# Kernel optimization log

Measured on AMD Instinct MI355X. Metric: run time of the kernel, lower is better.

## Reference

```python
import jax, jax.numpy as jnp
import numpy as np

BIAS = (1, 1)  # from init_kwargs

def setup_inputs() -> dict:
    key = jax.random.key(0)
    k1, k2 = jax.random.split(key)
    B, L = 32, 2048
    c = jax.random.normal(k1, (B, L), dtype=jnp.float32)
    y = jax.random.randint(k2, (B, L), 0, 2, dtype=jnp.int32)
    return {"c": c, "y": y}

def reference(c, y):
    # Faithful BP-MLL loss:
    # L = mean_i  (1 / (|Y_i|^b0 * |Ybar_i|^b1)) * sum_{k in Y_i, l in Ybar_i} exp(c_l - c_k)
    yf = (y == 1).astype(c.dtype)          # [B, L] positive-label mask
    y_bar = (y != 1).astype(c.dtype)       # [B, L] negative-label mask
    y_norm = jnp.sum(yf, axis=1) ** BIAS[0]
    y_bar_norm = jnp.sum(y_bar, axis=1) ** BIAS[1]
    # exp_matrix[b, k, l] = exp(c[b, l] - c[b, k]); masked pairwise sum
    exp_matrix = jnp.exp(c[:, None, :] - c[:, :, None])  # [B, L, L]
    pair = jnp.einsum('bk,bl,bkl->b', yf, y_bar, exp_matrix)
    return jnp.mean(pair / (y_norm * y_bar_norm))
```

## Files before the change

### kernel.cpp

```cpp
#include <hip/hip_runtime.h>


#define B_BATCH 32
#define L_LEN   2048

__global__ __launch_bounds__(256) void bpmll_row_kernel(
    const float* __restrict__ c,
    const int*   __restrict__ y,
    float*       __restrict__ row_out)
{
    const int b   = blockIdx.x;
    const int tid = threadIdx.x;
    const float* crow = c + (size_t)b * L_LEN;
    const int*   yrow = y + (size_t)b * L_LEN;

    float s_pos = 0.f;
    float s_neg = 0.f;
    float n_pos = 0.f;

    #pragma unroll
    for (int base = 0; base < L_LEN; base += 256 * 4) {
        const int i = base + tid * 4;
        const float4 cv = *reinterpret_cast<const float4*>(crow + i);
        const int4   yv = *reinterpret_cast<const int4*>(yrow + i);
        const float cc[4] = {cv.x, cv.y, cv.z, cv.w};
        const int   yy[4] = {yv.x, yv.y, yv.z, yv.w};
        #pragma unroll
        for (int j = 0; j < 4; ++j) {
            const bool pos = (yy[j] == 1);
            const float e = __expf(pos ? -cc[j] : cc[j]);
            if (pos) { s_pos += e; n_pos += 1.f; }
            else     { s_neg += e; }
        }
    }

    #pragma unroll
    for (int off = 32; off > 0; off >>= 1) {
        s_pos += __shfl_down(s_pos, off);
        s_neg += __shfl_down(s_neg, off);
        n_pos += __shfl_down(n_pos, off);
    }

    __shared__ float sm[3][4];
    const int wave = tid >> 6;
    const int lane = tid & 63;
    if (lane == 0) { sm[0][wave] = s_pos; sm[1][wave] = s_neg; sm[2][wave] = n_pos; }
    __syncthreads();

    if (tid == 0) {
        const float sp = sm[0][0] + sm[0][1] + sm[0][2] + sm[0][3];
        const float sn = sm[1][0] + sm[1][1] + sm[1][2] + sm[1][3];
        const float np = sm[2][0] + sm[2][1] + sm[2][2] + sm[2][3];
        const float nn = (float)L_LEN - np;
        row_out[b] = (sp * sn) / (np * nn);
    }
}

__global__ __launch_bounds__(64) void bpmll_final_kernel(
    const float* __restrict__ row_out,
    float*       __restrict__ out)
{
    const int tid = threadIdx.x;
    float v = (tid < B_BATCH) ? row_out[tid] : 0.f;
    #pragma unroll
    for (int off = 32; off > 0; off >>= 1) v += __shfl_down(v, off);
    if (tid == 0) out[0] = v * (1.0f / (float)B_BATCH);
}

extern "C" void kernel_launch(void* const* d_in, const int* in_sizes, int n_in,
                              void* d_out, int out_size, void* d_ws, size_t ws_size,
                              hipStream_t stream)
{
    const float* c = (const float*)d_in[0];
    const int*   y = (const int*)d_in[1];
    float* row = (float*)d_ws;
    float* out = (float*)d_out;

    bpmll_row_kernel<<<B_BATCH, 256, 0, stream>>>(c, y, row);
    bpmll_final_kernel<<<1, 64, 0, stream>>>(row, out);
}
```

Baseline: 56.06 us.

## Fuse row and final reduction into a single one-block kernel

Measured after the change: 60.17 us. 7.3% more time.

```diff
diff --git a/kernel.cpp b/kernel.cpp
--- a/kernel.cpp
+++ b/kernel.cpp
@@ -3,68 +3,70 @@
 
 #define B_BATCH 32
 #define L_LEN   2048
+#define NTHREADS 1024
+#define NWAVES  (NTHREADS / 64)
+#define ROWS_PER_WAVE (B_BATCH / NWAVES)
 
-__global__ __launch_bounds__(256) void bpmll_row_kernel(
+__global__ __launch_bounds__(NTHREADS) void bpmll_fused_kernel(
     const float* __restrict__ c,
     const int*   __restrict__ y,
-    float*       __restrict__ row_out)
+    float*       __restrict__ out)
 {
-    const int b   = blockIdx.x;
-    const int tid = threadIdx.x;
-    const float* crow = c + (size_t)b * L_LEN;
-    const int*   yrow = y + (size_t)b * L_LEN;
+    const int tid  = threadIdx.x;
+    const int wave = tid >> 6;
+    const int lane = tid & 63;
 
-    float s_pos = 0.f;
-    float s_neg = 0.f;
-    float n_pos = 0.f;
+    float acc = 0.f;
 
     #pragma unroll
-    for (int base = 0; base < L_LEN; base += 256 * 4) {
-        const int i = base + tid * 4;
-        const float4 cv = *reinterpret_cast<const float4*>(crow + i);
-        const int4   yv = *reinterpret_cast<const int4*>(yrow + i);
-        const float cc[4] = {cv.x, cv.y, cv.z, cv.w};
-        const int   yy[4] = {yv.x, yv.y, yv.z, yv.w};
+    for (int r = 0; r < ROWS_PER_WAVE; ++r) {
+        const int b = wave * ROWS_PER_WAVE + r;
+        const float* crow = c + (size_t)b * L_LEN;
+        const int*   yrow = y + (size_t)b * L_LEN;
+
+        float s_pos = 0.f;
+        float s_neg = 0.f;
+        float n_pos = 0.f;
+
         #pragma unroll
-        for (int j = 0; j < 4; ++j) {
-            const bool pos = (yy[j] == 1);
-            const float e = __expf(pos ? -cc[j] : cc[j]);
-            if (pos) { s_pos += e; n_pos += 1.f; }
-            else     { s_neg += e; }
+        for (int base = 0; base < L_LEN; base += 64 * 4) {
+            const int i = base + lane * 4;
+            const float4 cv = *reinterpret_cast<const float4*>(crow + i);
+            const int4   yv = *reinterpret_cast<const int4*>(yrow + i);
+            const float cc[4] = {cv.x, cv.y, cv.z, cv.w};
+            const int   yy[4] = {yv.x, yv.y, yv.z, yv.w};
+            #pragma unroll
+            for (int j = 0; j < 4; ++j) {
+                const bool pos = (yy[j] == 1);
+                const float e = __expf(pos ? -cc[j] : cc[j]);
+                if (pos) { s_pos += e; n_pos += 1.f; }
+                else     { s_neg += e; }
+            }
+        }
+
+        #pragma unroll
+        for (int off = 32; off > 0; off >>= 1) {
+            s_pos += __shfl_down(s_pos, off);
+            s_neg += __shfl_down(s_neg, off);
+            n_pos += __shfl_down(n_pos, off);
+        }
+
+        if (lane == 0) {
+            const float nn = (float)L_LEN - n_pos;
+            acc += (s_pos * s_neg) / (n_pos * nn);
         }
     }
 
-    #pragma unroll
-    for (int off = 32; off > 0; off >>= 1) {
-        s_pos += __shfl_down(s_pos, off);
-        s_neg += __shfl_down(s_neg, off);
-        n_pos += __shfl_down(n_pos, off);
-    }
-
-    __shared__ float sm[3][4];
-    const int wave = tid >> 6;
-    const int lane = tid & 63;
-    if (lane == 0) { sm[0][wave] = s_pos; sm[1][wave] = s_neg; sm[2][wave] = n_pos; }
+    __shared__ float sm[NWAVES];
+    if (lane == 0) sm[wave] = acc;
     __syncthreads();
 
     if (tid == 0) {
-        const float sp = sm[0][0] + sm[0][1] + sm[0][2] + sm[0][3];
-        const float sn = sm[1][0] + sm[1][1] + sm[1][2] + sm[1][3];
-        const float np = sm[2][0] + sm[2][1] + sm[2][2] + sm[2][3];
-        const float nn = (float)L_LEN - np;
-        row_out[b] = (sp * sn) / (np * nn);
+        float v = 0.f;
+        #pragma unroll
+        for (int w = 0; w < NWAVES; ++w) v += sm[w];
+        out[0] = v * (1.0f / (float)B_BATCH);
     }
-}
-
-__global__ __launch_bounds__(64) void bpmll_final_kernel(
-    const float* __restrict__ row_out,
-    float*       __restrict__ out)
-{
-    const int tid = threadIdx.x;
-    float v = (tid < B_BATCH) ? row_out[tid] : 0.f;
-    #pragma unroll
-    for (int off = 32; off > 0; off >>= 1) v += __shfl_down(v, off);
-    if (tid == 0) out[0] = v * (1.0f / (float)B_BATCH);
 }
 
 extern "C" void kernel_launch(void* const* d_in, const int* in_sizes, int n_in,
@@ -73,9 +75,7 @@
 {
     const float* c = (const float*)d_in[0];
     const int*   y = (const int*)d_in[1];
-    float* row = (float*)d_ws;
     float* out = (float*)d_out;
 
-    bpmll_row_kernel<<<B_BATCH, 256, 0, stream>>>(c, y, row);
-    bpmll_final_kernel<<<1, 64, 0, stream>>>(row, out);
+    bpmll_fused_kernel<<<1, NTHREADS, 0, stream>>>(c, y, out);
 }
```

## Fuse per-row and final reduction into one kernel with flag spin-wait

Applied to the files above, without the earlier changes.

After: 55.59 us. No clear change (-0.8%).

```diff
diff --git a/kernel.cpp b/kernel.cpp
--- a/kernel.cpp
+++ b/kernel.cpp
@@ -1,13 +1,17 @@
 #include <hip/hip_runtime.h>
+#include <stdint.h>
 
 
 #define B_BATCH 32
 #define L_LEN   2048
+#define NTHREADS 256
+#define MAGIC   0x5ca1ab1eu
 
-__global__ __launch_bounds__(256) void bpmll_row_kernel(
+__global__ __launch_bounds__(NTHREADS) void bpmll_onepass_kernel(
     const float* __restrict__ c,
     const int*   __restrict__ y,
-    float*       __restrict__ row_out)
+    float*       __restrict__ out,
+    uint32_t*    __restrict__ ws)
 {
     const int b   = blockIdx.x;
     const int tid = threadIdx.x;
@@ -18,13 +22,17 @@
     float s_neg = 0.f;
     float n_pos = 0.f;
 
+    float4 cv[2]; int4 yv[2];
     #pragma unroll
-    for (int base = 0; base < L_LEN; base += 256 * 4) {
-        const int i = base + tid * 4;
-        const float4 cv = *reinterpret_cast<const float4*>(crow + i);
-        const int4   yv = *reinterpret_cast<const int4*>(yrow + i);
-        const float cc[4] = {cv.x, cv.y, cv.z, cv.w};
-        const int   yy[4] = {yv.x, yv.y, yv.z, yv.w};
+    for (int it = 0; it < 2; ++it) {
+        const int i = it * NTHREADS * 4 + tid * 4;
+        cv[it] = *reinterpret_cast<const float4*>(crow + i);
+        yv[it] = *reinterpret_cast<const int4*>(yrow + i);
+    }
+    #pragma unroll
+    for (int it = 0; it < 2; ++it) {
+        const float cc[4] = {cv[it].x, cv[it].y, cv[it].z, cv[it].w};
+        const int   yy[4] = {yv[it].x, yv[it].y, yv[it].z, yv[it].w};
         #pragma unroll
         for (int j = 0; j < 4; ++j) {
             const bool pos = (yy[j] == 1);
@@ -52,19 +60,22 @@
         const float sn = sm[1][0] + sm[1][1] + sm[1][2] + sm[1][3];
         const float np = sm[2][0] + sm[2][1] + sm[2][2] + sm[2][3];
         const float nn = (float)L_LEN - np;
-        row_out[b] = (sp * sn) / (np * nn);
+        const float term = (sp * sn) / (np * nn);
+        __hip_atomic_store(&ws[b], __float_as_uint(term),
+                           __ATOMIC_RELAXED, __HIP_MEMORY_SCOPE_AGENT);
+        __hip_atomic_store(&ws[B_BATCH + b], MAGIC,
+                           __ATOMIC_RELEASE, __HIP_MEMORY_SCOPE_AGENT);
     }
-}
 
-__global__ __launch_bounds__(64) void bpmll_final_kernel(
-    const float* __restrict__ row_out,
-    float*       __restrict__ out)
-{
-    const int tid = threadIdx.x;
-    float v = (tid < B_BATCH) ? row_out[tid] : 0.f;
-    #pragma unroll
-    for (int off = 32; off > 0; off >>= 1) v += __shfl_down(v, off);
-    if (tid == 0) out[0] = v * (1.0f / (float)B_BATCH);
+    if (b == 0 && tid < B_BATCH) {
+        while (__hip_atomic_load(&ws[B_BATCH + tid],
+                                 __ATOMIC_ACQUIRE, __HIP_MEMORY_SCOPE_AGENT) != MAGIC) {}
+        float v = __uint_as_float(__hip_atomic_load(&ws[tid],
+                                  __ATOMIC_RELAXED, __HIP_MEMORY_SCOPE_AGENT));
+        #pragma unroll
+        for (int off = 16; off > 0; off >>= 1) v += __shfl_down(v, off);
+        if (tid == 0) out[0] = v * (1.0f / (float)B_BATCH);
+    }
 }
 
 extern "C" void kernel_launch(void* const* d_in, const int* in_sizes, int n_in,
@@ -73,9 +84,7 @@
 {
     const float* c = (const float*)d_in[0];
     const int*   y = (const int*)d_in[1];
-    float* row = (float*)d_ws;
-    float* out = (float*)d_out;
 
-    bpmll_row_kernel<<<B_BATCH, 256, 0, stream>>>(c, y, row);
-    bpmll_final_kernel<<<1, 64, 0, stream>>>(row, out);
+    bpmll_onepass_kernel<<<B_BATCH, NTHREADS, 0, stream>>>(
+        c, y, (float*)d_out, (uint32_t*)d_ws);
 }
```
